# Kernel tuning notes

Measured on AMD Instinct MI355X. Metric: run time of the kernel, lower is better.

The kernel has to match this reference:

```python
import jax, jax.numpy as jnp
import numpy as np

V, E, H, K, B, T = 50000, 256, 256, 9, 128, 512


def lstm_dir(x, lens, Wih, Whh, b):
    # x: [B,T,E] -> h outputs [B,T,H], packed-sequence semantics:
    # state frozen and outputs zeroed for t >= lens[b].
    Bs, Ts, _ = x.shape
    Hh = Whh.shape[1]
    xw = jnp.einsum('bte,ge->btg', x, Wih) + b  # [B,T,4H] precomputed input proj
    valid = jnp.arange(Ts)[None, :] < lens[:, None]  # [B,T]

    def step(carry, inp):
        h, c = carry
        xw_t, v = inp  # [B,4H], [B]
        gates = xw_t + h @ Whh.T
        i, f, g, o = jnp.split(gates, 4, axis=-1)  # torch gate order i,f,g,o
        i = jax.nn.sigmoid(i)
        f = jax.nn.sigmoid(f)
        g = jnp.tanh(g)
        o = jax.nn.sigmoid(o)
        c_new = f * c + i * g
        h_new = o * jnp.tanh(c_new)
        v = v[:, None]
        return (jnp.where(v, h_new, h), jnp.where(v, c_new, c)), h_new * v

    init = (jnp.zeros((Bs, Hh), x.dtype), jnp.zeros((Bs, Hh), x.dtype))
    _, ys = jax.lax.scan(step, init, (jnp.swapaxes(xw, 0, 1), valid.T))
    return jnp.swapaxes(ys, 0, 1)


def reverse_by_len(x, lens):
    # per-row reversal within valid length; padding stays zero
    Ts = x.shape[1]
    t = jnp.arange(Ts)
    idx = jnp.clip(lens[:, None] - 1 - t[None, :], 0, Ts - 1)
    m = t[None, :] < lens[:, None]
    return jnp.take_along_axis(x, idx[:, :, None], axis=1) * m[:, :, None]


def crf_llh(em, tags, lens, start, end, trans):
    # torchcrf forward with reduction='sum': sum_b (gold score - logZ)
    Bs, Ts, Kk = em.shape
    mask = jnp.arange(Ts)[None, :] < lens[:, None]
    em_t = jnp.take_along_axis(em, tags[..., None], axis=-1)[..., 0]  # [B,T]
    score = start[tags[:, 0]] + em_t[:, 0]
    tr = trans[tags[:, :-1], tags[:, 1:]]  # [B,T-1]
    score = score + jnp.sum((tr + em_t[:, 1:]) * mask[:, 1:], axis=1)
    last_tag = jnp.take_along_axis(tags, (lens - 1)[:, None], axis=1)[:, 0]
    score = score + end[last_tag]

    def step(alpha, inp):
        e_t, m_t = inp  # [B,K], [B]
        nxt = jax.nn.logsumexp(alpha[:, :, None] + trans[None, :, :], axis=1) + e_t
        return jnp.where(m_t[:, None], nxt, alpha), None

    alpha0 = start[None, :] + em[:, 0]  # [B,K]
    alpha, _ = jax.lax.scan(step, alpha0,
                            (jnp.swapaxes(em[:, 1:], 0, 1), mask[:, 1:].T))
    logZ = jax.nn.logsumexp(alpha + end[None, :], axis=1)
    return jnp.sum(score - logZ)


def setup_inputs() -> dict:
    key = jax.random.key(0)
    ks = jax.random.split(key, 16)
    sentences = jax.random.randint(ks[0], (B, T), 0, V)
    tags = jax.random.randint(ks[1], (B, T), 0, K)
    length_list = jax.random.randint(ks[2], (B,), 1, T + 1)  # >=1 so mask[:,0] all true
    s = float(1.0 / np.sqrt(H))
    u = lambda k, sh: jax.random.uniform(k, sh, jnp.float32, -s, s)
    emb = jax.random.normal(ks[3], (V, E), jnp.float32) * float(np.sqrt(2.0 / E))
    return dict(
        sentences=sentences, tags=tags, length_list=length_list,
        emb=emb,
        Wih_f=u(ks[4], (4 * H, E)), Whh_f=u(ks[5], (4 * H, H)), b_f=u(ks[6], (4 * H,)),
        Wih_b=u(ks[7], (4 * H, E)), Whh_b=u(ks[8], (4 * H, H)), b_b=u(ks[9], (4 * H,)),
        W_out=u(ks[10], (K, 2 * H)), b_out=u(ks[11], (K,)),
        start=jax.random.uniform(ks[12], (K,), jnp.float32, -0.1, 0.1),
        end=jax.random.uniform(ks[13], (K,), jnp.float32, -0.1, 0.1),
        trans=jax.random.uniform(ks[14], (K, K), jnp.float32, -0.1, 0.1),
    )


def reference(sentences, tags, length_list, emb, Wih_f, Whh_f, b_f,
              Wih_b, Whh_b, b_b, W_out, b_out, start, end, trans):
    x = emb[sentences]  # [B,T,E]
    h_f = lstm_dir(x, length_list, Wih_f, Whh_f, b_f)
    x_rev = reverse_by_len(x, length_list)
    h_b = reverse_by_len(lstm_dir(x_rev, length_list, Wih_b, Whh_b, b_b), length_list)
    hcat = jnp.concatenate([h_f, h_b], axis=-1)  # [B,T,2H]
    # Dropout is identity in eval mode
    em = jnp.einsum('bth,kh->btk', hcat, W_out) + b_out  # [B,T,K]
    return crf_llh(em, tags, length_list, start, end, trans)
```

## Files before the change

### kernel.cpp

```cpp
#include <hip/hip_runtime.h>
#include <hip/hip_bf16.h>

typedef short v8s __attribute__((ext_vector_type(8)));
typedef int   v8i __attribute__((ext_vector_type(8)));
typedef float v4f __attribute__((ext_vector_type(4)));
typedef float v2f __attribute__((ext_vector_type(2)));

#define T_ 512

__device__ __forceinline__ unsigned short f2bf(float f){
  unsigned int u = __builtin_bit_cast(unsigned int, f);
  unsigned int r = (u + 0x7fffu + ((u>>16)&1u)) >> 16;
  return (unsigned short)r;
}
template<int HI>
__device__ __forceinline__ v2f cvt2(unsigned int wsrc){
  return __builtin_amdgcn_cvt_pk_f32_fp8((int)wsrc, HI);
}
__device__ __forceinline__ float tanh_p(float x){
  float x2 = x*x;
  float num = x*(27.f + x2);
  float r = num * __builtin_amdgcn_rcpf(27.f + 9.f*x2);
  return fminf(fmaxf(r, -1.f), 1.f);
}
__device__ __forceinline__ float sigm_p(float x){
  return 0.5f + 0.5f*tanh_p(0.5f*x);
}
__device__ __forceinline__ int pi_col(int p){
  return ((p>>5)<<5) + ((p&1)<<4) + ((p&31)>>1);
}
__device__ __forceinline__ v8i ld32(const void* p){
  uint4 lo = *(const uint4*)p;
  uint4 hi = *(const uint4*)((const char*)p + 16);
  v8i r;
  r[0]=(int)lo.x; r[1]=(int)lo.y; r[2]=(int)lo.z; r[3]=(int)lo.w;
  r[4]=(int)hi.x; r[5]=(int)hi.y; r[6]=(int)hi.z; r[7]=(int)hi.w;
  return r;
}

__global__ __launch_bounds__(256) void prep_frag_k(
    const float* __restrict__ Wa, const float* __restrict__ Wb,
    unsigned short* __restrict__ out, int Ntot)
{
  int idx = blockIdx.x*256 + threadIdx.x;
  int lane = idx & 63;
  int t2 = idx >> 6;
  int ntiles = Ntot >> 4;
  int ntile = t2 % ntiles;
  int kt = t2 / ntiles;
  if (kt >= 8) return;
  int n  = ntile*16 + (lane & 15);
  int ks = lane >> 4;
  const float* src = (n < 1024) ? (Wa + (size_t)n*256) : (Wb + (size_t)(n-1024)*256);
  int k0 = kt*32 + ks*8;
  unsigned short* d = out + (size_t)idx*8;
  #pragma unroll
  for (int e=0;e<8;++e) d[e] = f2bf(src[k0+e]);
}

__global__ __launch_bounds__(256) void prep_whh8_k(
    const float* __restrict__ Wf, const float* __restrict__ Wb,
    unsigned char* __restrict__ out)
{
  int idx = blockIdx.x*256 + threadIdx.x;
  int lane = idx & 63;
  int t2 = idx >> 6;
  int ntile = t2 & 63;
  int kt = (t2>>6) & 1;
  int dir = t2 >> 7;
  const float* W = dir ? Wb : Wf;
  int n = ntile*16 + (lane&15);
  int kbase = kt*128 + (lane>>4)*32;
  const float* row = W + (size_t)n*256;
  unsigned words[8];
  #pragma unroll
  for (int e=0;e<8;++e){
    float v0 = row[pi_col(kbase + e*4 + 0)];
    float v1 = row[pi_col(kbase + e*4 + 1)];
    float v2 = row[pi_col(kbase + e*4 + 2)];
    float v3 = row[pi_col(kbase + e*4 + 3)];
    int w0 = __builtin_amdgcn_cvt_pk_fp8_f32(v0, v1, 0, 0);
    w0     = __builtin_amdgcn_cvt_pk_fp8_f32(v2, v3, w0, 1);
    words[e] = (unsigned)w0;
  }
  unsigned char* d = out + (size_t)idx*32;
  *(uint4*)(d)      = make_uint4(words[0], words[1], words[2], words[3]);
  *(uint4*)(d + 16) = make_uint4(words[4], words[5], words[6], words[7]);
}

__global__ __launch_bounds__(256) void xw_gemm_k(
    const int* __restrict__ sent, const float* __restrict__ emb,
    const unsigned short* __restrict__ wihg, const int* __restrict__ lens,
    unsigned char* __restrict__ xw)
{
  int mt = blockIdx.x;
  if (((mt&7)<<6) >= lens[mt>>3]) return;
  __shared__ unsigned short A[64][264];
  int tid = threadIdx.x;
  {
    int r = tid>>2, q = tid&3;
    int tok = sent[mt*64 + r];
    const float4* s = (const float4*)(emb + (size_t)tok*256 + q*64);
    unsigned short* drow = &A[r][q*64];
    #pragma unroll
    for (int cc=0; cc<16; ++cc){
      float4 v = s[cc];
      uint2 o;
      o.x = (unsigned)f2bf(v.x) | ((unsigned)f2bf(v.y)<<16);
      o.y = (unsigned)f2bf(v.z) | ((unsigned)f2bf(v.w)<<16);
      *(uint2*)(drow + cc*4) = o;
    }
  }
  __syncthreads();
  int w = tid>>6, lane = tid&63, lr = lane&15, lq = lane>>4;
  #pragma unroll 1
  for (int p=0;p<2;++p){
    int wv = w + p*4;
    #pragma unroll 1
    for (int dn=0;dn<2;++dn){
      v4f acc[8][4];
      #pragma unroll
      for (int e=0;e<8;++e)
        #pragma unroll
        for (int m=0;m<4;++m) acc[e][m] = (v4f){0.f,0.f,0.f,0.f};
      #pragma unroll
      for (int kt=0;kt<8;++kt){
        v8s a0 = *(const v8s*)(&A[ 0+lr][kt*32 + lq*8]);
        v8s a1 = *(const v8s*)(&A[16+lr][kt*32 + lq*8]);
        v8s a2 = *(const v8s*)(&A[32+lr][kt*32 + lq*8]);
        v8s a3 = *(const v8s*)(&A[48+lr][kt*32 + lq*8]);
        #pragma unroll
        for (int e=0;e<8;++e){
          int ntile = dn*64 + (e>>1)*16 + wv*2 + (e&1);
          v8s bfr = *(const v8s*)(wihg + ((size_t)(kt*128 + ntile)*64 + lane)*8);
          acc[e][0] = __builtin_amdgcn_mfma_f32_16x16x32_bf16(a0, bfr, acc[e][0], 0,0,0);
          acc[e][1] = __builtin_amdgcn_mfma_f32_16x16x32_bf16(a1, bfr, acc[e][1], 0,0,0);
          acc[e][2] = __builtin_amdgcn_mfma_f32_16x16x32_bf16(a2, bfr, acc[e][2], 0,0,0);
          acc[e][3] = __builtin_amdgcn_mfma_f32_16x16x32_bf16(a3, bfr, acc[e][3], 0,0,0);
        }
      }
      #pragma unroll
      for (int m=0;m<4;++m){
        #pragma unroll
        for (int j=0;j<4;++j){
          int mr = mt*64 + m*16 + lq*4 + j;
          int w0 = __builtin_amdgcn_cvt_pk_fp8_f32(acc[0][m][j], acc[1][m][j], 0, 0);
          w0     = __builtin_amdgcn_cvt_pk_fp8_f32(acc[2][m][j], acc[3][m][j], w0, 1);
          int w1 = __builtin_amdgcn_cvt_pk_fp8_f32(acc[4][m][j], acc[5][m][j], 0, 0);
          w1     = __builtin_amdgcn_cvt_pk_fp8_f32(acc[6][m][j], acc[7][m][j], w1, 1);
          *(uint2*)(xw + ((size_t)dn*65536 + mr)*1024 + wv*128 + lr*8)
              = make_uint2((unsigned)w0, (unsigned)w1);
        }
      }
    }
  }
}

__global__ __launch_bounds__(512,2) void lstm_k(
    const unsigned char* __restrict__ xw,
    const unsigned char* __restrict__ whh8,
    const float* __restrict__ bfv, const float* __restrict__ bbv,
    const int* __restrict__ lens,
    unsigned char* __restrict__ hout)
{
  int bid = blockIdx.x, dir = bid>>5, grp = bid&31;
  int tid = threadIdx.x, w = tid>>6, lane = tid&63, lr = lane&15, lq = lane>>4;
  __shared__ unsigned char hbuf[2][16][272];
  __shared__ int tmax_s;
  for (int i=tid*4; i<2*16*272; i+=512*4) *(unsigned int*)(&((unsigned char*)hbuf)[i]) = 0u;
  if (tid==0){
    int mx=0;
    for (int i=0;i<4;++i){ int l = lens[grp*4+i]; mx = l>mx? l:mx; }
    tmax_s = mx;
  }
  v8i wreg[16];
  const unsigned char* wb = whh8 + (size_t)dir*262144;
  #pragma unroll
  for (int kt=0;kt<2;++kt){
    #pragma unroll
    for (int nt=0;nt<8;++nt){
      int ntile = (nt>>1)*16 + w*2 + (nt&1);
      wreg[kt*8+nt] = ld32(wb + ((size_t)(kt*64 + ntile)*64 + lane)*32);
    }
  }
  const float* bb = dir ? bbv : bfv;
  float bias[4][2];
  #pragma unroll
  for (int q=0;q<4;++q){
    bias[q][0] = bb[q*256 + w*32 + lr];
    bias[q][1] = bb[q*256 + w*32 + 16 + lr];
  }
  int seq = grp*4 + lq;
  int ln = lens[seq];
  float c0 = 0.f, c1 = 0.f;
  const size_t dbase = (size_t)dir*65536;
  const unsigned char* xbase = xw + (dbase + (size_t)seq*T_)*1024 + w*128 + lr*8;
  unsigned char* hbase = hout + (dbase + (size_t)seq*T_)*256 + w*32 + lr*2;
  __syncthreads();
  int tmax = tmax_s;
  uint2 xv = *(const uint2*)(xbase + (size_t)(dir ? (ln-1) : 0)*1024);
  for (int t=0; t<tmax; ++t){
    int cur = t&1, nxt = cur^1;
    int tn = (t+1<tmax)? t+1 : t;
    int te = (dir && tn<ln) ? (ln-1-tn) : tn;
    uint2 xn = *(const uint2*)(xbase + (size_t)te*1024);
    v4f acc[8];
    #pragma unroll
    for (int nt=0;nt<8;++nt) acc[nt] = (v4f){0.f,0.f,0.f,0.f};
    #pragma unroll
    for (int kt=0;kt<2;++kt){
      v8i a = ld32(&hbuf[cur][lr][kt*128 + lq*32]);
      #pragma unroll
      for (int nt=0;nt<8;++nt)
        acc[nt] = __builtin_amdgcn_mfma_scale_f32_16x16x128_f8f6f4(
                    a, wreg[kt*8+nt], acc[nt],
                    0, 0,
                    0, 0x7f7f7f7f,
                    0, 0x7f7f7f7f);
    }
    bool valid = t < ln;
    int pos = (dir && valid) ? (ln-1-t) : t;
    v2f xi = cvt2<0>(xv.x);
    v2f xf = cvt2<1>(xv.x);
    v2f xg = cvt2<0>(xv.y);
    v2f xo = cvt2<1>(xv.y);
    float hn0, hn1;
    {
      float gi = acc[0][0] + xi[0] + bias[0][0];
      float gf = acc[2][0] + xf[0] + bias[1][0];
      float gg = acc[4][0] + xg[0] + bias[2][0];
      float go = acc[6][0] + xo[0] + bias[3][0];
      float iv = sigm_p(gi), fv = sigm_p(gf), gv = tanh_p(gg), ov = sigm_p(go);
      float cn = fv*c0 + iv*gv;
      hn0 = ov*tanh_p(cn);
      if (valid) c0 = cn;
    }
    {
      float gi = acc[1][0] + xi[1] + bias[0][1];
      float gf = acc[3][0] + xf[1] + bias[1][1];
      float gg = acc[5][0] + xg[1] + bias[2][1];
      float go = acc[7][0] + xo[1] + bias[3][1];
      float iv = sigm_p(gi), fv = sigm_p(gf), gv = tanh_p(gg), ov = sigm_p(go);
      float cn = fv*c1 + iv*gv;
      hn1 = ov*tanh_p(cn);
      if (valid) c1 = cn;
    }
    int hp = __builtin_amdgcn_cvt_pk_fp8_f32(hn0, hn1, 0, 0);
    unsigned short hu = valid ? (unsigned short)(hp & 0xffff) : (unsigned short)0;
    if (valid)
      *(unsigned short*)(&hbuf[nxt][lq*4][w*32 + lr*2]) = hu;
    *(unsigned short*)(hbase + (size_t)pos*256) = hu;
    xv = xn;
    asm volatile("s_waitcnt lgkmcnt(0)" ::: "memory");
    __builtin_amdgcn_s_barrier();
    __builtin_amdgcn_sched_barrier(0);
  }
}

__global__ __launch_bounds__(256) void em_k(
    const unsigned char* __restrict__ hout,
    const float* __restrict__ Wout, const float* __restrict__ bout,
    const int* __restrict__ lens,
    float* __restrict__ em)
{
  __shared__ float Ws[9*512];
  for (int i=threadIdx.x;i<9*512;i+=256){
    int k = i>>9, p = i&511;
    int d = p>>8, pp = p&255;
    Ws[i] = Wout[k*512 + d*256 + pi_col(pp)];
  }
  __syncthreads();
  int wv = blockIdx.x*4 + (threadIdx.x>>6);
  int lane = threadIdx.x & 63;
  int g = lane>>4, r = lane&15;
  int m = wv*4 + g;
  const unsigned char* hf = hout + (size_t)m*256 + r*16;
  const unsigned char* hb = hout + ((size_t)65536 + m)*256 + r*16;
  uint4 vf = *(const uint4*)hf;
  uint4 vb = *(const uint4*)hb;
  float xf[16], xb[16];
  {
    v2f d0=cvt2<0>(vf.x), d1=cvt2<1>(vf.x), d2=cvt2<0>(vf.y), d3=cvt2<1>(vf.y);
    v2f d4=cvt2<0>(vf.z), d5=cvt2<1>(vf.z), d6=cvt2<0>(vf.w), d7=cvt2<1>(vf.w);
    xf[0]=d0.x; xf[1]=d0.y; xf[2]=d1.x; xf[3]=d1.y;
    xf[4]=d2.x; xf[5]=d2.y; xf[6]=d3.x; xf[7]=d3.y;
    xf[8]=d4.x; xf[9]=d4.y; xf[10]=d5.x; xf[11]=d5.y;
    xf[12]=d6.x; xf[13]=d6.y; xf[14]=d7.x; xf[15]=d7.y;
  }
  {
    v2f d0=cvt2<0>(vb.x), d1=cvt2<1>(vb.x), d2=cvt2<0>(vb.y), d3=cvt2<1>(vb.y);
    v2f d4=cvt2<0>(vb.z), d5=cvt2<1>(vb.z), d6=cvt2<0>(vb.w), d7=cvt2<1>(vb.w);
    xb[0]=d0.x; xb[1]=d0.y; xb[2]=d1.x; xb[3]=d1.y;
    xb[4]=d2.x; xb[5]=d2.y; xb[6]=d3.x; xb[7]=d3.y;
    xb[8]=d4.x; xb[9]=d4.y; xb[10]=d5.x; xb[11]=d5.y;
    xb[12]=d6.x; xb[13]=d6.y; xb[14]=d7.x; xb[15]=d7.y;
  }
  float a[9];
  #pragma unroll
  for (int k=0;k<9;++k){
    float s = 0.f;
    #pragma unroll
    for (int e=0;e<16;++e)
      s += xf[e]*Ws[k*512 + r*16 + e] + xb[e]*Ws[k*512 + 256 + r*16 + e];
    a[k]=s;
  }
  #pragma unroll
  for (int k=0;k<9;++k){
    #pragma unroll
    for (int off=8; off; off>>=1) a[k] += __shfl_xor(a[k], off, 64);
  }
  int b = m>>9, t = m&511;
  if (r==0 && t < lens[b]){
    float* d = em + (size_t)m*9;
    #pragma unroll
    for (int k=0;k<9;++k) d[k] = a[k] + bout[k];
  }
}

__global__ __launch_bounds__(256) void crf_k(
    const float* __restrict__ em, const int* __restrict__ tags,
    const int* __restrict__ lens, const float* __restrict__ startv,
    const float* __restrict__ endv, const float* __restrict__ trans,
    float* __restrict__ out)
{
  int wid = blockIdx.x*4 + (threadIdx.x>>6);
  int lane = threadIdx.x & 63;
  const float* e = em + (size_t)wid*T_*9;
  const int* tg = tags + (size_t)wid*T_;
  int L = lens[wid];
  float p = 0.f;
  for (int t = 1+lane; t < L; t += 64)
    p += trans[tg[t-1]*9 + tg[t]] + e[(size_t)t*9 + tg[t]];
  if (lane==0) p += startv[tg[0]] + e[tg[0]] + endv[tg[L-1]];
  #pragma unroll
  for (int off=32; off; off>>=1) p += __shfl_xor(p, off, 64);
  float tcol[9];
  #pragma unroll
  for (int i=0;i<9;++i) tcol[i] = (lane<9) ? trans[i*9 + lane] : 0.f;
  float alpha = (lane<9) ? (startv[lane] + e[lane]) : -1e30f;
  for (int t=1; t<L; ++t){
    float vs[9]; float mx = -1e30f;
    #pragma unroll
    for (int i=0;i<9;++i){
      float ai = __shfl(alpha, i, 64);
      vs[i] = ai + tcol[i];
      mx = fmaxf(mx, vs[i]);
    }
    float s = 0.f;
    #pragma unroll
    for (int i=0;i<9;++i) s += __expf(vs[i]-mx);
    float na = mx + __logf(s) + ((lane<9)? e[(size_t)t*9+lane] : 0.f);
    alpha = (lane<9) ? na : -1e30f;
  }
  float v = (lane<9) ? (alpha + endv[lane]) : -1e30f;
  float mx = v;
  #pragma unroll
  for (int off=32; off; off>>=1) mx = fmaxf(mx, __shfl_xor(mx, off, 64));
  float s = __expf(v-mx);
  #pragma unroll
  for (int off=32; off; off>>=1) s += __shfl_xor(s, off, 64);
  float logZ = mx + __logf(s);
  if (lane==0) atomicAdd(out, p - logZ);
}

extern "C" void kernel_launch(void* const* d_in, const int* in_sizes, int n_in,
                              void* d_out, int out_size, void* d_ws, size_t ws_size,
                              hipStream_t stream)
{
  const int*   sent  = (const int*)d_in[0];
  const int*   tags  = (const int*)d_in[1];
  const int*   lens  = (const int*)d_in[2];
  const float* emb   = (const float*)d_in[3];
  const float* Wih_f = (const float*)d_in[4];
  const float* Whh_f = (const float*)d_in[5];
  const float* b_f   = (const float*)d_in[6];
  const float* Wih_b = (const float*)d_in[7];
  const float* Whh_b = (const float*)d_in[8];
  const float* b_b   = (const float*)d_in[9];
  const float* Wout  = (const float*)d_in[10];
  const float* bout  = (const float*)d_in[11];
  const float* startv= (const float*)d_in[12];
  const float* endv  = (const float*)d_in[13];
  const float* trans = (const float*)d_in[14];
  char* ws = (char*)d_ws;
  unsigned short* wihg = (unsigned short*)(ws);
  unsigned char*  whh8 = (unsigned char*)(ws + (size_t)1048576);
  unsigned char*  xw   = (unsigned char*)(ws + (size_t)1572864);
  unsigned char*  hout = (unsigned char*)(ws + (size_t)135790592);
  float* em            = (float*)(ws + (size_t)169345024);
  float* outp = (float*)d_out;

  (void)hipMemsetAsync(outp, 0, sizeof(float), stream);
  prep_frag_k<<<256, 256, 0, stream>>>(Wih_f, Wih_b, wihg, 2048);
  prep_whh8_k<<<64, 256, 0, stream>>>(Whh_f, Whh_b, whh8);
  xw_gemm_k<<<1024, 256, 0, stream>>>(sent, emb, wihg, lens, xw);
  lstm_k<<<64, 512, 0, stream>>>(xw, whh8, b_f, b_b, lens, hout);
  em_k<<<4096, 256, 0, stream>>>(hout, Wout, bout, lens, em);
  crf_k<<<32, 256, 0, stream>>>(em, tags, lens, startv, endv, trans, outp);
}
```

Before: 842.7 us.

## Quantize Whh to FP4 and Wih/embeddings to FP8, fold bias into input projection

```diff
diff --git a/kernel.cpp b/kernel.cpp
--- a/kernel.cpp
+++ b/kernel.cpp
@@ -3,16 +3,12 @@
 
 typedef short v8s __attribute__((ext_vector_type(8)));
 typedef int   v8i __attribute__((ext_vector_type(8)));
+typedef int   v4i __attribute__((ext_vector_type(4)));
 typedef float v4f __attribute__((ext_vector_type(4)));
 typedef float v2f __attribute__((ext_vector_type(2)));
 
 #define T_ 512
 
-__device__ __forceinline__ unsigned short f2bf(float f){
-  unsigned int u = __builtin_bit_cast(unsigned int, f);
-  unsigned int r = (u + 0x7fffu + ((u>>16)&1u)) >> 16;
-  return (unsigned short)r;
-}
 template<int HI>
 __device__ __forceinline__ v2f cvt2(unsigned int wsrc){
   return __builtin_amdgcn_cvt_pk_f32_fp8((int)wsrc, HI);
@@ -37,28 +33,44 @@
   r[4]=(int)hi.x; r[5]=(int)hi.y; r[6]=(int)hi.z; r[7]=(int)hi.w;
   return r;
 }
-
-__global__ __launch_bounds__(256) void prep_frag_k(
+__device__ __forceinline__ unsigned f2fp4(float x){
+  unsigned s = (x < 0.f) ? 8u : 0u;
+  float a = fabsf(x);
+  unsigned m;
+  if      (a < 0.25f) m=0u; else if (a < 0.75f) m=1u;
+  else if (a < 1.25f) m=2u; else if (a < 1.75f) m=3u;
+  else if (a < 2.5f ) m=4u; else if (a < 3.5f ) m=5u;
+  else if (a < 5.f  ) m=6u; else m=7u;
+  return s|m;
+}
+__device__ __forceinline__ unsigned pk8(float a, float b, float c, float d){
+  int w = __builtin_amdgcn_cvt_pk_fp8_f32(a, b, 0, 0);
+  w     = __builtin_amdgcn_cvt_pk_fp8_f32(c, d, w, 1);
+  return (unsigned)w;
+}
+
+__global__ __launch_bounds__(256) void prep_wih8_k(
     const float* __restrict__ Wa, const float* __restrict__ Wb,
-    unsigned short* __restrict__ out, int Ntot)
+    unsigned char* __restrict__ out)
 {
   int idx = blockIdx.x*256 + threadIdx.x;
   int lane = idx & 63;
   int t2 = idx >> 6;
-  int ntiles = Ntot >> 4;
-  int ntile = t2 % ntiles;
-  int kt = t2 / ntiles;
-  if (kt >= 8) return;
-  int n  = ntile*16 + (lane & 15);
-  int ks = lane >> 4;
-  const float* src = (n < 1024) ? (Wa + (size_t)n*256) : (Wb + (size_t)(n-1024)*256);
-  int k0 = kt*32 + ks*8;
-  unsigned short* d = out + (size_t)idx*8;
-  #pragma unroll
-  for (int e=0;e<8;++e) d[e] = f2bf(src[k0+e]);
-}
-
-__global__ __launch_bounds__(256) void prep_whh8_k(
+  int ntile = t2 & 127;
+  int kt = t2 >> 7;
+  int n = ntile*16 + (lane&15);
+  const float* W = (n < 1024) ? (Wa + (size_t)n*256) : (Wb + (size_t)(n-1024)*256);
+  int k0 = kt*128 + (lane>>4)*32;
+  unsigned words[8];
+  #pragma unroll
+  for (int e=0;e<8;++e)
+    words[e] = pk8(W[k0+e*4], W[k0+e*4+1], W[k0+e*4+2], W[k0+e*4+3]);
+  unsigned char* d = out + (size_t)idx*32;
+  *(uint4*)(d)      = make_uint4(words[0], words[1], words[2], words[3]);
+  *(uint4*)(d + 16) = make_uint4(words[4], words[5], words[6], words[7]);
+}
+
+__global__ __launch_bounds__(256) void prep_whh4_k(
     const float* __restrict__ Wf, const float* __restrict__ Wb,
     unsigned char* __restrict__ out)
 {
@@ -72,84 +84,98 @@
   int n = ntile*16 + (lane&15);
   int kbase = kt*128 + (lane>>4)*32;
   const float* row = W + (size_t)n*256;
-  unsigned words[8];
-  #pragma unroll
-  for (int e=0;e<8;++e){
-    float v0 = row[pi_col(kbase + e*4 + 0)];
-    float v1 = row[pi_col(kbase + e*4 + 1)];
-    float v2 = row[pi_col(kbase + e*4 + 2)];
-    float v3 = row[pi_col(kbase + e*4 + 3)];
-    int w0 = __builtin_amdgcn_cvt_pk_fp8_f32(v0, v1, 0, 0);
-    w0     = __builtin_amdgcn_cvt_pk_fp8_f32(v2, v3, w0, 1);
-    words[e] = (unsigned)w0;
-  }
-  unsigned char* d = out + (size_t)idx*32;
-  *(uint4*)(d)      = make_uint4(words[0], words[1], words[2], words[3]);
-  *(uint4*)(d + 16) = make_uint4(words[4], words[5], words[6], words[7]);
+  unsigned words[4];
+  #pragma unroll
+  for (int d4=0;d4<4;++d4){
+    unsigned acc = 0;
+    #pragma unroll
+    for (int j=0;j<8;++j){
+      float v = row[pi_col(kbase + d4*8 + j)] * 64.f;
+      acc |= f2fp4(v) << (4*j);
+    }
+    words[d4] = acc;
+  }
+  *(uint4*)(out + (size_t)idx*16) = make_uint4(words[0], words[1], words[2], words[3]);
 }
 
 __global__ __launch_bounds__(256) void xw_gemm_k(
     const int* __restrict__ sent, const float* __restrict__ emb,
-    const unsigned short* __restrict__ wihg, const int* __restrict__ lens,
+    const unsigned char* __restrict__ wihg, const int* __restrict__ lens,
+    const float* __restrict__ bfv, const float* __restrict__ bbv,
     unsigned char* __restrict__ xw)
 {
   int mt = blockIdx.x;
-  if (((mt&7)<<6) >= lens[mt>>3]) return;
-  __shared__ unsigned short A[64][264];
+  if (((mt&3)<<7) >= lens[mt>>2]) return;
+  __shared__ unsigned char A[128][272];
   int tid = threadIdx.x;
   {
-    int r = tid>>2, q = tid&3;
-    int tok = sent[mt*64 + r];
-    const float4* s = (const float4*)(emb + (size_t)tok*256 + q*64);
-    unsigned short* drow = &A[r][q*64];
-    #pragma unroll
-    for (int cc=0; cc<16; ++cc){
-      float4 v = s[cc];
-      uint2 o;
-      o.x = (unsigned)f2bf(v.x) | ((unsigned)f2bf(v.y)<<16);
-      o.y = (unsigned)f2bf(v.z) | ((unsigned)f2bf(v.w)<<16);
-      *(uint2*)(drow + cc*4) = o;
+    int row = tid>>1, half = tid&1;
+    int tok = sent[mt*128 + row];
+    const float4* s = (const float4*)(emb + (size_t)tok*256 + half*128);
+    unsigned char* drow = &A[row][half*128];
+    #pragma unroll
+    for (int c4=0; c4<8; ++c4){
+      unsigned w0[4];
+      #pragma unroll
+      for (int u=0; u<4; ++u){
+        float4 v = s[c4*4+u];
+        w0[u] = pk8(v.x, v.y, v.z, v.w);
+      }
+      *(uint4*)(drow + c4*16) = make_uint4(w0[0], w0[1], w0[2], w0[3]);
     }
   }
   __syncthreads();
   int w = tid>>6, lane = tid&63, lr = lane&15, lq = lane>>4;
   #pragma unroll 1
-  for (int p=0;p<2;++p){
-    int wv = w + p*4;
+  for (int i4=0; i4<4; ++i4){
+    int dnv = w*4 + i4;
+    int dn = dnv>>3, v = dnv&7;
+    const float* bb = dn ? bbv : bfv;
+    float bias[8];
+    #pragma unroll
+    for (int e=0;e<8;++e){
+      int q = e>>1, s = e&1;
+      bias[e] = bb[q*256 + v*32 + s*16 + lr];
+    }
     #pragma unroll 1
-    for (int dn=0;dn<2;++dn){
+    for (int mh=0; mh<2; ++mh){
       v4f acc[8][4];
       #pragma unroll
       for (int e=0;e<8;++e)
         #pragma unroll
-        for (int m=0;m<4;++m) acc[e][m] = (v4f){0.f,0.f,0.f,0.f};
+        for (int mm=0;mm<4;++mm) acc[e][mm] = (v4f){0.f,0.f,0.f,0.f};
       #pragma unroll
-      for (int kt=0;kt<8;++kt){
-        v8s a0 = *(const v8s*)(&A[ 0+lr][kt*32 + lq*8]);
-        v8s a1 = *(const v8s*)(&A[16+lr][kt*32 + lq*8]);
-        v8s a2 = *(const v8s*)(&A[32+lr][kt*32 + lq*8]);
-        v8s a3 = *(const v8s*)(&A[48+lr][kt*32 + lq*8]);
+      for (int kt=0;kt<2;++kt){
+        v8i a0 = ld32(&A[mh*64 +  0 + lr][kt*128 + lq*32]);
+        v8i a1 = ld32(&A[mh*64 + 16 + lr][kt*128 + lq*32]);
+        v8i a2 = ld32(&A[mh*64 + 32 + lr][kt*128 + lq*32]);
+        v8i a3 = ld32(&A[mh*64 + 48 + lr][kt*128 + lq*32]);
         #pragma unroll
         for (int e=0;e<8;++e){
-          int ntile = dn*64 + (e>>1)*16 + wv*2 + (e&1);
-          v8s bfr = *(const v8s*)(wihg + ((size_t)(kt*128 + ntile)*64 + lane)*8);
-          acc[e][0] = __builtin_amdgcn_mfma_f32_16x16x32_bf16(a0, bfr, acc[e][0], 0,0,0);
-          acc[e][1] = __builtin_amdgcn_mfma_f32_16x16x32_bf16(a1, bfr, acc[e][1], 0,0,0);
-          acc[e][2] = __builtin_amdgcn_mfma_f32_16x16x32_bf16(a2, bfr, acc[e][2], 0,0,0);
-          acc[e][3] = __builtin_amdgcn_mfma_f32_16x16x32_bf16(a3, bfr, acc[e][3], 0,0,0);
+          int q = e>>1, s = e&1;
+          int ntile = dn*64 + q*16 + v*2 + s;
+          v8i bfr = ld32(wihg + ((size_t)(kt*128 + ntile)*64 + lane)*32);
+          acc[e][0] = __builtin_amdgcn_mfma_scale_f32_16x16x128_f8f6f4(
+                        a0, bfr, acc[e][0], 0,0, 0,0x7f7f7f7f, 0,0x7f7f7f7f);
+          acc[e][1] = __builtin_amdgcn_mfma_scale_f32_16x16x128_f8f6f4(
+                        a1, bfr, acc[e][1], 0,0, 0,0x7f7f7f7f, 0,0x7f7f7f7f);
+          acc[e][2] = __builtin_amdgcn_mfma_scale_f32_16x16x128_f8f6f4(
+                        a2, bfr, acc[e][2], 0,0, 0,0x7f7f7f7f, 0,0x7f7f7f7f);
+          acc[e][3] = __builtin_amdgcn_mfma_scale_f32_16x16x128_f8f6f4(
+                        a3, bfr, acc[e][3], 0,0, 0,0x7f7f7f7f, 0,0x7f7f7f7f);
         }
       }
       #pragma unroll
-      for (int m=0;m<4;++m){
+      for (int mm=0;mm<4;++mm){
         #pragma unroll
         for (int j=0;j<4;++j){
-          int mr = mt*64 + m*16 + lq*4 + j;
-          int w0 = __builtin_amdgcn_cvt_pk_fp8_f32(acc[0][m][j], acc[1][m][j], 0, 0);
-          w0     = __builtin_amdgcn_cvt_pk_fp8_f32(acc[2][m][j], acc[3][m][j], w0, 1);
-          int w1 = __builtin_amdgcn_cvt_pk_fp8_f32(acc[4][m][j], acc[5][m][j], 0, 0);
-          w1     = __builtin_amdgcn_cvt_pk_fp8_f32(acc[6][m][j], acc[7][m][j], w1, 1);
-          *(uint2*)(xw + ((size_t)dn*65536 + mr)*1024 + wv*128 + lr*8)
-              = make_uint2((unsigned)w0, (unsigned)w1);
+          int row = mt*128 + mh*64 + mm*16 + lq*4 + j;
+          unsigned lo = pk8(acc[0][mm][j]+bias[0], acc[1][mm][j]+bias[1],
+                            acc[2][mm][j]+bias[2], acc[3][mm][j]+bias[3]);
+          unsigned hi = pk8(acc[4][mm][j]+bias[4], acc[5][mm][j]+bias[5],
+                            acc[6][mm][j]+bias[6], acc[7][mm][j]+bias[7]);
+          *(uint2*)(xw + ((size_t)dn*65536 + row)*1024 + v*128 + lr*8)
+              = make_uint2(lo, hi);
         }
       }
     }
@@ -158,8 +184,7 @@
 
 __global__ __launch_bounds__(512,2) void lstm_k(
     const unsigned char* __restrict__ xw,
-    const unsigned char* __restrict__ whh8,
-    const float* __restrict__ bfv, const float* __restrict__ bbv,
+    const unsigned char* __restrict__ whh4,
     const int* __restrict__ lens,
     unsigned char* __restrict__ hout)
 {
@@ -173,22 +198,17 @@
     for (int i=0;i<4;++i){ int l = lens[grp*4+i]; mx = l>mx? l:mx; }
     tmax_s = mx;
   }
-  v8i wreg[16];
-  const unsigned char* wb = whh8 + (size_t)dir*262144;
+  v4i wreg[16];
+  const unsigned char* wb = whh4 + (size_t)dir*131072;
   #pragma unroll
   for (int kt=0;kt<2;++kt){
     #pragma unroll
     for (int nt=0;nt<8;++nt){
       int ntile = (nt>>1)*16 + w*2 + (nt&1);
-      wreg[kt*8+nt] = ld32(wb + ((size_t)(kt*64 + ntile)*64 + lane)*32);
-    }
-  }
-  const float* bb = dir ? bbv : bfv;
-  float bias[4][2];
-  #pragma unroll
-  for (int q=0;q<4;++q){
-    bias[q][0] = bb[q*256 + w*32 + lr];
-    bias[q][1] = bb[q*256 + w*32 + 16 + lr];
+      uint4 t = *(const uint4*)(wb + ((size_t)(kt*64 + ntile)*64 + lane)*16);
+      v4i r; r[0]=(int)t.x; r[1]=(int)t.y; r[2]=(int)t.z; r[3]=(int)t.w;
+      wreg[kt*8+nt] = r;
+    }
   }
   int seq = grp*4 + lq;
   int ln = lens[seq];
@@ -211,12 +231,16 @@
     for (int kt=0;kt<2;++kt){
       v8i a = ld32(&hbuf[cur][lr][kt*128 + lq*32]);
       #pragma unroll
-      for (int nt=0;nt<8;++nt)
+      for (int nt=0;nt<8;++nt){
+        v4i wv4 = wreg[kt*8+nt];
+        v8i b; b[0]=wv4[0]; b[1]=wv4[1]; b[2]=wv4[2]; b[3]=wv4[3];
+        b[4]=0; b[5]=0; b[6]=0; b[7]=0;
         acc[nt] = __builtin_amdgcn_mfma_scale_f32_16x16x128_f8f6f4(
-                    a, wreg[kt*8+nt], acc[nt],
-                    0, 0,
+                    a, b, acc[nt],
+                    0, 4,
                     0, 0x7f7f7f7f,
-                    0, 0x7f7f7f7f);
+                    0, 0x79797979);
+      }
     }
     bool valid = t < ln;
     int pos = (dir && valid) ? (ln-1-t) : t;
@@ -226,20 +250,20 @@
     v2f xo = cvt2<1>(xv.y);
     float hn0, hn1;
     {
-      float gi = acc[0][0] + xi[0] + bias[0][0];
-      float gf = acc[2][0] + xf[0] + bias[1][0];
-      float gg = acc[4][0] + xg[0] + bias[2][0];
-      float go = acc[6][0] + xo[0] + bias[3][0];
+      float gi = acc[0][0] + xi[0];
+      float gf = acc[2][0] + xf[0];
+      float gg = acc[4][0] + xg[0];
+      float go = acc[6][0] + xo[0];
       float iv = sigm_p(gi), fv = sigm_p(gf), gv = tanh_p(gg), ov = sigm_p(go);
       float cn = fv*c0 + iv*gv;
       hn0 = ov*tanh_p(cn);
       if (valid) c0 = cn;
     }
     {
-      float gi = acc[1][0] + xi[1] + bias[0][1];
-      float gf = acc[3][0] + xf[1] + bias[1][1];
-      float gg = acc[5][0] + xg[1] + bias[2][1];
-      float go = acc[7][0] + xo[1] + bias[3][1];
+      float gi = acc[1][0] + xi[1];
+      float gf = acc[3][0] + xf[1];
+      float gg = acc[5][0] + xg[1];
+      float go = acc[7][0] + xo[1];
       float iv = sigm_p(gi), fv = sigm_p(gf), gv = tanh_p(gg), ov = sigm_p(go);
       float cn = fv*c1 + iv*gv;
       hn1 = ov*tanh_p(cn);
@@ -383,18 +407,18 @@
   const float* endv  = (const float*)d_in[13];
   const float* trans = (const float*)d_in[14];
   char* ws = (char*)d_ws;
-  unsigned short* wihg = (unsigned short*)(ws);
-  unsigned char*  whh8 = (unsigned char*)(ws + (size_t)1048576);
-  unsigned char*  xw   = (unsigned char*)(ws + (size_t)1572864);
-  unsigned char*  hout = (unsigned char*)(ws + (size_t)135790592);
-  float* em            = (float*)(ws + (size_t)169345024);
+  unsigned char* wihg8 = (unsigned char*)(ws);
+  unsigned char* whh4  = (unsigned char*)(ws + (size_t)524288);
+  unsigned char* xw    = (unsigned char*)(ws + (size_t)1048576);
+  unsigned char* hout  = (unsigned char*)(ws + (size_t)135266304);
+  float* em            = (float*)(ws + (size_t)168820736);
   float* outp = (float*)d_out;
 
   (void)hipMemsetAsync(outp, 0, sizeof(float), stream);
-  prep_frag_k<<<256, 256, 0, stream>>>(Wih_f, Wih_b, wihg, 2048);
-  prep_whh8_k<<<64, 256, 0, stream>>>(Whh_f, Whh_b, whh8);
-  xw_gemm_k<<<1024, 256, 0, stream>>>(sent, emb, wihg, lens, xw);
-  lstm_k<<<64, 512, 0, stream>>>(xw, whh8, b_f, b_b, lens, hout);
+  prep_wih8_k<<<64, 256, 0, stream>>>(Wih_f, Wih_b, wihg8);
+  prep_whh4_k<<<64, 256, 0, stream>>>(Whh_f, Whh_b, whh4);
+  xw_gemm_k<<<512, 256, 0, stream>>>(sent, emb, wihg8, lens, b_f, b_b, xw);
+  lstm_k<<<64, 512, 0, stream>>>(xw, whh4, lens, hout);
   em_k<<<4096, 256, 0, stream>>>(hout, Wout, bout, lens, em);
   crf_k<<<32, 256, 0, stream>>>(em, tags, lens, startv, endv, trans, outp);
 }
```

Result: faster. 744.2 us (-11.7%).
